# Kernel tuning notes

Hardware: AMD Instinct MI355X
Metric: run time of the kernel (lower is better)

## Reference

```python
import jax, jax.numpy as jnp
import numpy as np

N = 200000
HID = 256
HEADS = 8
HD = HID // HEADS
C = 1000  # num clusters


def setup_inputs() -> dict:
    key = jax.random.key(0)
    ks = jax.random.split(key, 8)
    s = 1.0 / np.sqrt(HID)
    return {
        "x": jax.random.normal(ks[0], (N, HID), dtype=jnp.float32),
        "cluster_assignments": jax.random.randint(ks[1], (N,), 0, C),
        "batch": jnp.zeros((N,), dtype=jnp.int64),
        "Wk": jax.random.uniform(ks[2], (HID, HID), minval=-s, maxval=s),
        "bk": jnp.zeros((HID,), dtype=jnp.float32),
        "Wv": jax.random.uniform(ks[3], (HID, HID), minval=-s, maxval=s),
        "bv": jnp.zeros((HID,), dtype=jnp.float32),
        "Wo": jax.random.uniform(ks[4], (HID, HID), minval=-s, maxval=s),
        "bo": jnp.zeros((HID,), dtype=jnp.float32),
        "pool_query": jax.random.normal(ks[5], (1, HEADS, HD), dtype=jnp.float32),
    }


def reference(x, cluster_assignments, batch, Wk, bk, Wv, bv, Wo, bo, pool_query):
    seg = cluster_assignments
    scale = HD ** -0.5
    keys = (x @ Wk.T + bk).reshape(-1, HEADS, HD)     # [N, H, D]
    values = (x @ Wv.T + bv).reshape(-1, HEADS, HD)   # [N, H, D]
    # attention scores per node/head against shared pool query
    scores = jnp.einsum('nhd,hd->nh', keys, pool_query[0]) * scale  # [N, H]
    # segment-wise (per-cluster) softmax over nodes, per head
    m = jax.ops.segment_max(scores, seg, num_segments=C)            # [C, H]
    e = jnp.exp(scores - m[seg])                                    # [N, H]
    z = jax.ops.segment_sum(e, seg, num_segments=C)                 # [C, H]
    w = e / z[seg]                                                  # [N, H]
    attended = (w[..., None] * values).reshape(-1, HID)             # [N, HID]
    # scatter_mean over clusters
    ssum = jax.ops.segment_sum(attended, seg, num_segments=C)       # [C, HID]
    cnt = jax.ops.segment_sum(jnp.ones((attended.shape[0],), attended.dtype), seg, num_segments=C)
    pooled = ssum / jnp.clip(cnt, 1.0)[:, None]                     # [C, HID]
    out = pooled @ Wo.T + bo                                        # [C, HID]
    return out[seg]                                                 # [N, HID]
```

## Files before the change

### kernel.cpp

```cpp
#include <hip/hip_runtime.h>
#include <math.h>

#define HID 256
#define HEADS 8
#define HD 32
#define C_CLUST 1000
#define SCALEQ 0.17677669529663687f
#define CAP 512
#define NW 8
#define SCORE_BLOCKS 2048

typedef float fx4 __attribute__((ext_vector_type(4)));

__global__ __launch_bounds__(256) void k_prep(const float* __restrict__ Wk,
                                              const float* __restrict__ bk,
                                              const float* __restrict__ pq,
                                              float* __restrict__ qk,
                                              float* __restrict__ cb,
                                              int* __restrict__ cur) {
  __shared__ float qv[HD];
  int h = blockIdx.x;
  int t = threadIdx.x;
  int g = h * 256 + t;
  for (int i = g; i < C_CLUST; i += 2048) cur[i] = 0;
  if (t < HD) qv[t] = pq[h * HD + t];
  __syncthreads();
  float a = 0.f;
#pragma unroll 8
  for (int d = 0; d < HD; ++d) a += Wk[(size_t)(h * HD + d) * HID + t] * qv[d];
  qk[h * HID + t] = a * SCALEQ;
  if (t == 0) {
    float s = 0.f;
    for (int d = 0; d < HD; ++d) s += bk[h * HD + d] * qv[d];
    cb[h] = s * SCALEQ;
  }
}

__global__ __launch_bounds__(256) void k_scores(const float* __restrict__ x,
                                                const int* __restrict__ seg,
                                                const float* __restrict__ qk,
                                                const float* __restrict__ cb,
                                                float* __restrict__ es,
                                                int* __restrict__ cur,
                                                int* __restrict__ list, int N) {
  int l = threadIdx.x & 63;
  int wv = (int)(((size_t)blockIdx.x * blockDim.x + threadIdx.x) >> 6);
  int nwv = (int)(((size_t)gridDim.x * blockDim.x) >> 6);
  int strip = (N + nwv - 1) / nwv;
  int n0 = wv * strip;
  int n1 = n0 + strip;
  if (n1 > N) n1 = N;
  float4 q4[8];
#pragma unroll
  for (int h = 0; h < 8; ++h) q4[h] = *(const float4*)(qk + h * HID + 4 * l);
  float cbv = cb[l & 7];
#pragma unroll 2
  for (int n = n0; n < n1; ++n) {
    float4 xv = *(const float4*)(x + (size_t)n * HID + 4 * l);
    float r0 = xv.x * q4[0].x + xv.y * q4[0].y + xv.z * q4[0].z + xv.w * q4[0].w;
    float r1 = xv.x * q4[1].x + xv.y * q4[1].y + xv.z * q4[1].z + xv.w * q4[1].w;
    float r2 = xv.x * q4[2].x + xv.y * q4[2].y + xv.z * q4[2].z + xv.w * q4[2].w;
    float r3 = xv.x * q4[3].x + xv.y * q4[3].y + xv.z * q4[3].z + xv.w * q4[3].w;
    float r4 = xv.x * q4[4].x + xv.y * q4[4].y + xv.z * q4[4].z + xv.w * q4[4].w;
    float r5 = xv.x * q4[5].x + xv.y * q4[5].y + xv.z * q4[5].z + xv.w * q4[5].w;
    float r6 = xv.x * q4[6].x + xv.y * q4[6].y + xv.z * q4[6].z + xv.w * q4[6].w;
    float r7 = xv.x * q4[7].x + xv.y * q4[7].y + xv.z * q4[7].z + xv.w * q4[7].w;
    r0 += __shfl_xor(r0, 1); r0 += __shfl_xor(r0, 2); r0 += __shfl_xor(r0, 4);
    r1 += __shfl_xor(r1, 1); r1 += __shfl_xor(r1, 2); r1 += __shfl_xor(r1, 4);
    r2 += __shfl_xor(r2, 1); r2 += __shfl_xor(r2, 2); r2 += __shfl_xor(r2, 4);
    r3 += __shfl_xor(r3, 1); r3 += __shfl_xor(r3, 2); r3 += __shfl_xor(r3, 4);
    r4 += __shfl_xor(r4, 1); r4 += __shfl_xor(r4, 2); r4 += __shfl_xor(r4, 4);
    r5 += __shfl_xor(r5, 1); r5 += __shfl_xor(r5, 2); r5 += __shfl_xor(r5, 4);
    r6 += __shfl_xor(r6, 1); r6 += __shfl_xor(r6, 2); r6 += __shfl_xor(r6, 4);
    r7 += __shfl_xor(r7, 1); r7 += __shfl_xor(r7, 2); r7 += __shfl_xor(r7, 4);
    int p = l & 7;
    float v = (p < 4) ? ((p < 2) ? (p == 0 ? r0 : r1) : (p == 2 ? r2 : r3))
                      : ((p < 6) ? (p == 4 ? r4 : r5) : (p == 6 ? r6 : r7));
    v += __shfl_xor(v, 8); v += __shfl_xor(v, 16); v += __shfl_xor(v, 32);
    v += cbv;
    if (l < 8) es[(size_t)n * 8 + l] = __expf(v);
    if (l == 0) {
      int c = seg[n];
      int pos = atomicAdd(&cur[c], 1);
      if (pos < CAP) list[c * CAP + pos] = n;
    }
  }
}

__global__ __launch_bounds__(512) void k_pool(const float* __restrict__ x,
                                              const float* __restrict__ es,
                                              const int* __restrict__ cur,
                                              const int* __restrict__ list,
                                              const float* __restrict__ Wv,
                                              const float* __restrict__ bv,
                                              const float* __restrict__ Wo,
                                              const float* __restrict__ bo,
                                              float* __restrict__ outc) {
  __shared__ float4 buf4[512];
  __shared__ float s_lds[8 * HID];
  __shared__ float red[NW * 8];
  __shared__ float p_lds[HID];
  int c = blockIdx.x;
  int t = threadIdx.x;
  int cnt = cur[c];
  if (cnt == 0) return;
  int cntL = (cnt < CAP) ? cnt : CAP;
  int w = t >> 6, l = t & 63;
  const int* lp = list + c * CAP;

  float4 acc[8];
#pragma unroll
  for (int h = 0; h < 8; ++h) acc[h] = make_float4(0.f, 0.f, 0.f, 0.f);
  float zacc[8];
#pragma unroll
  for (int h = 0; h < 8; ++h) zacc[h] = 0.f;
  const float* xb = x + 4 * l;

#define ROW(NI)                                                                \
  { int nn = (NI);                                                             \
    float4 ea = *(const float4*)(es + (size_t)nn * 8);                         \
    float4 eb4 = *(const float4*)(es + (size_t)nn * 8 + 4);                    \
    float4 xv = *(const float4*)(xb + (size_t)nn * HID);                       \
    float eh[8] = {ea.x, ea.y, ea.z, ea.w, eb4.x, eb4.y, eb4.z, eb4.w};        \
    _Pragma("unroll")                                                          \
    for (int h = 0; h < 8; ++h) {                                              \
      acc[h].x += eh[h] * xv.x; acc[h].y += eh[h] * xv.y;                      \
      acc[h].z += eh[h] * xv.z; acc[h].w += eh[h] * xv.w;                      \
      zacc[h] += eh[h]; } }
  int i = w;
  for (; i + 7 * NW < cntL; i += 8 * NW) {
    int n0 = lp[i],          n1 = lp[i + NW],     n2 = lp[i + 2 * NW],
        n3 = lp[i + 3 * NW], n4 = lp[i + 4 * NW], n5 = lp[i + 5 * NW],
        n6 = lp[i + 6 * NW], n7 = lp[i + 7 * NW];
    ROW(n0) ROW(n1) ROW(n2) ROW(n3) ROW(n4) ROW(n5) ROW(n6) ROW(n7)
  }
  for (; i < cntL; i += NW) ROW(lp[i])
#undef ROW

#pragma unroll
  for (int h = 0; h < 8; ++h)
    if (l == h) red[w * 8 + h] = zacc[h];
  __syncthreads();
  float zinv[8];
#pragma unroll
  for (int h = 0; h < 8; ++h) {
    float z = 0.f;
#pragma unroll
    for (int w2 = 0; w2 < NW; ++w2) z += red[w2 * 8 + h];
    zinv[h] = (z > 0.f) ? 1.f / z : 0.f;
  }

#pragma unroll
  for (int h = 0; h < 8; ++h) {
    __syncthreads();
    buf4[t] = acc[h];
    __syncthreads();
    if (t < 64) {
      float4 s = buf4[t];
#pragma unroll
      for (int w2 = 1; w2 < NW; ++w2) {
        float4 b = buf4[w2 * 64 + t];
        s.x += b.x; s.y += b.y; s.z += b.z; s.w += b.w;
      }
      float sc = zinv[h];
      s.x *= sc; s.y *= sc; s.z *= sc; s.w *= sc;
      *(float4*)&s_lds[h * HID + 4 * t] = s;
    }
  }
  __syncthreads();

  int grp = t >> 2, q = t & 3;
  float rc = 1.f / (float)cnt;
#pragma unroll
  for (int r = 0; r < 2; ++r) {
    int o = grp + 128 * r;
    const float4* wr = (const float4*)(Wv + (size_t)o * HID);
    const float4* sr = (const float4*)(s_lds + (o >> 5) * HID);
    float a = 0.f;
#pragma unroll
    for (int k = 0; k < 16; ++k) {
      float4 w4 = wr[q + 4 * k];
      float4 s4 = sr[q + 4 * k];
      a += w4.x * s4.x + w4.y * s4.y + w4.z * s4.z + w4.w * s4.w;
    }
    a += __shfl_xor(a, 1);
    a += __shfl_xor(a, 2);
    if (q == 0) p_lds[o] = (a + bv[o]) * rc;
  }
  __syncthreads();
#pragma unroll
  for (int r = 0; r < 2; ++r) {
    int o = grp + 128 * r;
    const float4* wr = (const float4*)(Wo + (size_t)o * HID);
    const float4* pr = (const float4*)p_lds;
    float a = 0.f;
#pragma unroll
    for (int k = 0; k < 16; ++k) {
      float4 w4 = wr[q + 4 * k];
      float4 p4 = pr[q + 4 * k];
      a += w4.x * p4.x + w4.y * p4.y + w4.z * p4.z + w4.w * p4.w;
    }
    a += __shfl_xor(a, 1);
    a += __shfl_xor(a, 2);
    if (q == 0) outc[(size_t)c * HID + o] = a + bo[o];
  }
}

__global__ __launch_bounds__(256) void k_expand(const int* __restrict__ seg,
                                                const float* __restrict__ outc,
                                                float* __restrict__ out, int N) {
  size_t g = (size_t)blockIdx.x * blockDim.x + threadIdx.x;
  size_t total = (size_t)N * (HID / 4);
  size_t stride = (size_t)gridDim.x * blockDim.x;
  const float4* oc = (const float4*)outc;
  float4* o4 = (float4*)out;
  for (; g < total; g += stride) {
    int n = (int)(g >> 6);
    int q = (int)(g & 63);
    int c = seg[n];
    o4[g] = oc[(size_t)c * 64 + q];
  }
}

extern "C" void kernel_launch(void* const* d_in, const int* in_sizes, int n_in,
                              void* d_out, int out_size, void* d_ws, size_t ws_size,
                              hipStream_t stream) {
  const float* x = (const float*)d_in[0];
  const int* seg = (const int*)d_in[1];
  const float* Wk = (const float*)d_in[3];
  const float* bk = (const float*)d_in[4];
  const float* Wv = (const float*)d_in[5];
  const float* bv = (const float*)d_in[6];
  const float* Wo = (const float*)d_in[7];
  const float* bo = (const float*)d_in[8];
  const float* pq = (const float*)d_in[9];
  int N = in_sizes[0] / HID;

  char* ws = (char*)d_ws;
  size_t cur_off = 0;
  auto take = [&](size_t bytes) -> void* {
    void* p = ws + cur_off;
    cur_off += (bytes + 255) & ~(size_t)255;
    return p;
  };
  float* qk = (float*)take((size_t)HEADS * HID * 4);
  float* cb = (float*)take((size_t)HEADS * 4);
  int* cur = (int*)take((size_t)C_CLUST * 4);
  int* list = (int*)take((size_t)C_CLUST * CAP * 4);
  float* es = (float*)take((size_t)N * 8 * 4);
  float* outc = (float*)take((size_t)C_CLUST * HID * 4);

  k_prep<<<HEADS, 256, 0, stream>>>(Wk, bk, pq, qk, cb, cur);
  k_scores<<<SCORE_BLOCKS, 256, 0, stream>>>(x, seg, qk, cb, es, cur, list, N);
  k_pool<<<C_CLUST, 512, 0, stream>>>(x, es, cur, list, Wv, bv, Wo, bo, outc);
  k_expand<<<2048, 256, 0, stream>>>(seg, outc, (float*)d_out, N);
}
```

Measured before the change: 207.0 us.

## Process 8-row tiles per wave with butterfly transpose reduction in score kernel

```diff
diff --git a/kernel.cpp b/kernel.cpp
--- a/kernel.cpp
+++ b/kernel.cpp
@@ -8,7 +8,6 @@
 #define SCALEQ 0.17677669529663687f
 #define CAP 512
 #define NW 8
-#define SCORE_BLOCKS 2048
 
 typedef float fx4 __attribute__((ext_vector_type(4)));
 
@@ -46,45 +45,80 @@
   int l = threadIdx.x & 63;
   int wv = (int)(((size_t)blockIdx.x * blockDim.x + threadIdx.x) >> 6);
   int nwv = (int)(((size_t)gridDim.x * blockDim.x) >> 6);
-  int strip = (N + nwv - 1) / nwv;
-  int n0 = wv * strip;
-  int n1 = n0 + strip;
-  if (n1 > N) n1 = N;
   float4 q4[8];
 #pragma unroll
   for (int h = 0; h < 8; ++h) q4[h] = *(const float4*)(qk + h * HID + 4 * l);
   float cbv = cb[l & 7];
-#pragma unroll 2
-  for (int n = n0; n < n1; ++n) {
-    float4 xv = *(const float4*)(x + (size_t)n * HID + 4 * l);
-    float r0 = xv.x * q4[0].x + xv.y * q4[0].y + xv.z * q4[0].z + xv.w * q4[0].w;
-    float r1 = xv.x * q4[1].x + xv.y * q4[1].y + xv.z * q4[1].z + xv.w * q4[1].w;
-    float r2 = xv.x * q4[2].x + xv.y * q4[2].y + xv.z * q4[2].z + xv.w * q4[2].w;
-    float r3 = xv.x * q4[3].x + xv.y * q4[3].y + xv.z * q4[3].z + xv.w * q4[3].w;
-    float r4 = xv.x * q4[4].x + xv.y * q4[4].y + xv.z * q4[4].z + xv.w * q4[4].w;
-    float r5 = xv.x * q4[5].x + xv.y * q4[5].y + xv.z * q4[5].z + xv.w * q4[5].w;
-    float r6 = xv.x * q4[6].x + xv.y * q4[6].y + xv.z * q4[6].z + xv.w * q4[6].w;
-    float r7 = xv.x * q4[7].x + xv.y * q4[7].y + xv.z * q4[7].z + xv.w * q4[7].w;
-    r0 += __shfl_xor(r0, 1); r0 += __shfl_xor(r0, 2); r0 += __shfl_xor(r0, 4);
-    r1 += __shfl_xor(r1, 1); r1 += __shfl_xor(r1, 2); r1 += __shfl_xor(r1, 4);
-    r2 += __shfl_xor(r2, 1); r2 += __shfl_xor(r2, 2); r2 += __shfl_xor(r2, 4);
-    r3 += __shfl_xor(r3, 1); r3 += __shfl_xor(r3, 2); r3 += __shfl_xor(r3, 4);
-    r4 += __shfl_xor(r4, 1); r4 += __shfl_xor(r4, 2); r4 += __shfl_xor(r4, 4);
-    r5 += __shfl_xor(r5, 1); r5 += __shfl_xor(r5, 2); r5 += __shfl_xor(r5, 4);
-    r6 += __shfl_xor(r6, 1); r6 += __shfl_xor(r6, 2); r6 += __shfl_xor(r6, 4);
-    r7 += __shfl_xor(r7, 1); r7 += __shfl_xor(r7, 2); r7 += __shfl_xor(r7, 4);
-    int p = l & 7;
-    float v = (p < 4) ? ((p < 2) ? (p == 0 ? r0 : r1) : (p == 2 ? r2 : r3))
-                      : ((p < 6) ? (p == 4 ? r4 : r5) : (p == 6 ? r6 : r7));
-    v += __shfl_xor(v, 8); v += __shfl_xor(v, 16); v += __shfl_xor(v, 32);
-    v += cbv;
-    if (l < 8) es[(size_t)n * 8 + l] = __expf(v);
-    if (l == 0) {
-      int c = seg[n];
-      int pos = atomicAdd(&cur[c], 1);
-      if (pos < CAP) list[c * CAP + pos] = n;
-    }
-  }
+  bool b0 = (l & 1) != 0, b1 = (l & 2) != 0, b2 = (l & 4) != 0;
+  int hsel = l >> 3;
+  int ntile = (N + 7) >> 3;
+
+#define ROWSCORE(XV, OUT)                                                      \
+  { float r0 = XV.x * q4[0].x + XV.y * q4[0].y + XV.z * q4[0].z + XV.w * q4[0].w; \
+    float r1 = XV.x * q4[1].x + XV.y * q4[1].y + XV.z * q4[1].z + XV.w * q4[1].w; \
+    float r2 = XV.x * q4[2].x + XV.y * q4[2].y + XV.z * q4[2].z + XV.w * q4[2].w; \
+    float r3 = XV.x * q4[3].x + XV.y * q4[3].y + XV.z * q4[3].z + XV.w * q4[3].w; \
+    float r4 = XV.x * q4[4].x + XV.y * q4[4].y + XV.z * q4[4].z + XV.w * q4[4].w; \
+    float r5 = XV.x * q4[5].x + XV.y * q4[5].y + XV.z * q4[5].z + XV.w * q4[5].w; \
+    float r6 = XV.x * q4[6].x + XV.y * q4[6].y + XV.z * q4[6].z + XV.w * q4[6].w; \
+    float r7 = XV.x * q4[7].x + XV.y * q4[7].y + XV.z * q4[7].z + XV.w * q4[7].w; \
+    float t0 = (b0 ? r1 : r0) + __shfl_xor(b0 ? r0 : r1, 1);                   \
+    float t1 = (b0 ? r3 : r2) + __shfl_xor(b0 ? r2 : r3, 1);                   \
+    float t2 = (b0 ? r5 : r4) + __shfl_xor(b0 ? r4 : r5, 1);                   \
+    float t3 = (b0 ? r7 : r6) + __shfl_xor(b0 ? r6 : r7, 1);                   \
+    float u0 = (b1 ? t1 : t0) + __shfl_xor(b1 ? t0 : t1, 2);                   \
+    float u1 = (b1 ? t3 : t2) + __shfl_xor(b1 ? t2 : t3, 2);                   \
+    float gg = (b2 ? u1 : u0) + __shfl_xor(b2 ? u0 : u1, 4);                   \
+    gg += __shfl_xor(gg, 8);                                                   \
+    gg += __shfl_xor(gg, 16);                                                  \
+    gg += __shfl_xor(gg, 32);                                                  \
+    OUT = gg; }
+
+  for (int tile = wv; tile < ntile; tile += nwv) {
+    int n0 = tile * 8;
+    float f0, f1, f2, f3, f4, f5, f6, f7;
+    if (n0 + 8 <= N) {
+      const float* xb = x + (size_t)n0 * HID + 4 * l;
+      float4 xv0 = *(const float4*)(xb + 0 * HID);
+      float4 xv1 = *(const float4*)(xb + 1 * HID);
+      float4 xv2 = *(const float4*)(xb + 2 * HID);
+      float4 xv3 = *(const float4*)(xb + 3 * HID);
+      float4 xv4 = *(const float4*)(xb + 4 * HID);
+      float4 xv5 = *(const float4*)(xb + 5 * HID);
+      float4 xv6 = *(const float4*)(xb + 6 * HID);
+      float4 xv7 = *(const float4*)(xb + 7 * HID);
+      ROWSCORE(xv0, f0) ROWSCORE(xv1, f1) ROWSCORE(xv2, f2) ROWSCORE(xv3, f3)
+      ROWSCORE(xv4, f4) ROWSCORE(xv5, f5) ROWSCORE(xv6, f6) ROWSCORE(xv7, f7)
+      float fs = (hsel < 4)
+                     ? ((hsel < 2) ? (hsel == 0 ? f0 : f1) : (hsel == 2 ? f2 : f3))
+                     : ((hsel < 6) ? (hsel == 4 ? f4 : f5) : (hsel == 6 ? f6 : f7));
+      es[(size_t)n0 * 8 + l] = __expf(fs + cbv);
+      if (l < 8) {
+        int row = n0 + l;
+        int c = seg[row];
+        int pos = atomicAdd(&cur[c], 1);
+        if (pos < CAP) list[c * CAP + pos] = row;
+      }
+    } else {
+      float fr[1];
+      for (int j = 0; j < 8; ++j) {
+        int n = n0 + j;
+        float4 xv = make_float4(0.f, 0.f, 0.f, 0.f);
+        if (n < N) xv = *(const float4*)(x + (size_t)n * HID + 4 * l);
+        ROWSCORE(xv, fr[0])
+        if (n < N) {
+          float v = fr[0] + cbv;
+          if (l < 8) es[(size_t)n * 8 + l] = __expf(v);
+          if (l == 0) {
+            int c = seg[n];
+            int pos = atomicAdd(&cur[c], 1);
+            if (pos < CAP) list[c * CAP + pos] = n;
+          }
+        }
+      }
+    }
+  }
+#undef ROWSCORE
 }
 
 __global__ __launch_bounds__(512) void k_pool(const float* __restrict__ x,
@@ -251,7 +285,9 @@
   float* outc = (float*)take((size_t)C_CLUST * HID * 4);
 
   k_prep<<<HEADS, 256, 0, stream>>>(Wk, bk, pq, qk, cb, cur);
-  k_scores<<<SCORE_BLOCKS, 256, 0, stream>>>(x, seg, qk, cb, es, cur, list, N);
+  int ntile = (N + 7) / 8;
+  int sb = (ntile + 3) / 4;
+  k_scores<<<sb, 256, 0, stream>>>(x, seg, qk, cb, es, cur, list, N);
   k_pool<<<C_CLUST, 512, 0, stream>>>(x, es, cur, list, Wv, bv, Wo, bo, outc);
   k_expand<<<2048, 256, 0, stream>>>(seg, outc, (float*)d_out, N);
 }
```

New measurement: 191.8 us. 1.08x faster.
